# Performance work log

Measured on AMD Instinct MI355X. Metric: run time of the kernel, lower is better.

Reference implementation:

```python
import jax, jax.numpy as jnp
import numpy as np

EMG_SAMPLE_RATE = 2000
ROLLOUT_FREQ = 50
LEFT_CTX = 32
RIGHT_CTX = 32
NUM_POSITION_STEPS = 2000  # in EMG samples
OUT_CH = 20


def _interp_linear(x, size, align_corners):
    """x: [..., L] -> [..., size]; matches torch F.interpolate(mode='linear')."""
    L = x.shape[-1]
    if align_corners:
        src = jnp.arange(size, dtype=jnp.float32) * ((L - 1) / max(size - 1, 1))
    else:
        src = (jnp.arange(size, dtype=jnp.float32) + 0.5) * (L / size) - 0.5
        src = jnp.clip(src, 0.0, L - 1)
    lo = jnp.floor(src).astype(jnp.int32)
    hi = jnp.minimum(lo + 1, L - 1)
    w = (src - lo.astype(jnp.float32)).astype(x.dtype)
    return x[..., lo] * (1 - w) + x[..., hi] * w


def setup_inputs() -> dict:
    key = jax.random.key(0)
    ks = jax.random.split(key, 8)
    B, C, T = 32, 16, 8000
    F, K, H = 512, 65, 512
    emg = jax.random.normal(ks[0], (B, C, T), jnp.float32)
    joint_angles = jax.random.normal(ks[1], (B, OUT_CH, T), jnp.float32)
    no_ik_failure = jnp.ones((B, T), dtype=bool)
    conv_w = jax.random.normal(ks[2], (F, C, K), jnp.float32) * 0.05
    conv_b = jnp.zeros((F,), jnp.float32)
    w1 = jax.random.normal(ks[3], (F + OUT_CH, H), jnp.float32) * 0.04
    b1 = jnp.zeros((H,), jnp.float32)
    w2 = jax.random.normal(ks[4], (H, 2 * OUT_CH), jnp.float32) * 0.04
    b2 = jnp.zeros((2 * OUT_CH,), jnp.float32)
    return dict(emg=emg, joint_angles=joint_angles, no_ik_failure=no_ik_failure,
                provide_initial_pos=1, conv_w=conv_w, conv_b=conv_b,
                w1=w1, b1=b1, w2=w2, b2=b2)


def reference(emg, joint_angles, no_ik_failure, provide_initial_pos,
              conv_w, conv_b, w1, b1, w2, b2):
    B, _, T = emg.shape
    initial_pos = joint_angles[:, :, LEFT_CTX]
    if not provide_initial_pos:
        initial_pos = jnp.zeros_like(initial_pos)

    # encoder: valid Conv1d -> [B, F, T - K + 1] = [B, F, T - 64]
    feats = jax.lax.conv_general_dilated(
        emg, conv_w, window_strides=(1,), padding='VALID',
        dimension_numbers=('NCH', 'OIH', 'NCH')) + conv_b[None, :, None]

    seconds = (T - LEFT_CTX - RIGHT_CTX) / EMG_SAMPLE_RATE
    n_time = round(seconds * ROLLOUT_FREQ)          # static python int
    feats = _interp_linear(feats, n_time, align_corners=True)  # [B, F, n_time]
    num_pos_steps = round(NUM_POSITION_STEPS * (ROLLOUT_FREQ / EMG_SAMPLE_RATE))

    feats_t = jnp.transpose(feats, (2, 0, 1))  # [n_time, B, F]

    def step(prev, inp):
        x_t, t = inp
        # state_condition=True: concat previous pose prediction
        h = jax.nn.relu(jnp.concatenate([x_t, prev], axis=-1) @ w1 + b1)
        out = h @ w2 + b2                       # [B, 2*OUT_CH]
        pos, vel = out[:, :OUT_CH], out[:, OUT_CH:]
        pred = jnp.where(t < num_pos_steps, pos, prev + vel)
        return pred, pred

    _, preds = jax.lax.scan(step, initial_pos,
                            (feats_t, jnp.arange(n_time)))
    pred = jnp.transpose(preds, (1, 2, 0))  # [B, OUT_CH, n_time]

    ja = joint_angles[:, :, LEFT_CTX:T - RIGHT_CTX]
    mask = no_ik_failure[:, LEFT_CTX:T - RIGHT_CTX]
    nt = ja.shape[-1]
    pred_up = _interp_linear(pred, nt, align_corners=False)
    # nearest resample of mask to its own length is identity
    return pred_up, ja, mask
```

## Files before the change

### kernel.cpp

```cpp
#include <hip/hip_runtime.h>

#define NT   198
#define BB   32
#define CC   16
#define TT   8000
#define FF   512
#define KW   65
#define HD   512
#define OUT  20
#define CJ   (CC*KW)
#define KP   1056
#define MM   (NT*BB)
#define TOUT 7936
#define NPS  50

typedef float f4 __attribute__((ext_vector_type(4)));

#define WS_CW 0
#define WS_BX (WS_CW + KP*HD)
#define WS_X  (WS_BX + HD)
#define WS_PR (WS_X  + MM*HD)
#define WS_ET (WS_PR + MM*OUT)
#define WS_W2T (WS_ET + KP*MM)

__device__ __forceinline__ void gll16(const float* g, float* l) {
    __builtin_amdgcn_global_load_lds(
        (const __attribute__((address_space(1))) unsigned int*)g,
        (__attribute__((address_space(3))) unsigned int*)l,
        16, 0, 0);
}

#define XBAR() do { asm volatile("s_waitcnt lgkmcnt(0)" ::: "memory"); \
                    __builtin_amdgcn_s_barrier(); } while (0)

#define ESPAN 2688
#define NB_E  (3 * (BB * CC + 4))
#define NB_CW (((KP + 63) / 64) * (HD / 64))
__global__ __launch_bounds__(256) void k_pre(const float* __restrict__ emg,
                                             const float* __restrict__ cwraw,
                                             const float* __restrict__ w1,
                                             const float* __restrict__ conv_b,
                                             const float* __restrict__ b1,
                                             const float* __restrict__ w2,
                                             float* __restrict__ Et,
                                             float* __restrict__ CW,
                                             float* __restrict__ bX,
                                             float* __restrict__ w2t) {
    __shared__ float sh[2 * 32 * 68];
    const int bid = blockIdx.x;
    const int tid = threadIdx.x;

    if (bid < NB_E) {
        const int bx = bid % (BB * CC + 4);
        const int tc = bid / (BB * CC + 4);
        if (bx >= BB * CC) {
            int idx = (bx - BB * CC) * 3 + tc;
            f4* zp = (f4*)(Et + (size_t)CJ * MM);
            f4 z = {0.f, 0.f, 0.f, 0.f};
            for (int j = tid; j < 2112; j += 256) zp[(size_t)idx * 2112 + j] = z;
            return;
        }
        float* lds_e = sh;
        const int bq = bx >> 4, c = bx & 15;
        const int t0 = tc * 66;
        const float CSTEP = 7935.0f / 197.0f;
        const int elo0 = (int)floorf((float)t0 * CSTEP);
        const float* erow = emg + (size_t)(bq * CC + c) * TT;
        for (int i = tid; i < ESPAN; i += 256) {
            int g = elo0 + i;
            lds_e[i] = erow[(g < TT) ? g : (TT - 1)];
        }
        __syncthreads();
        for (int o = tid; o < 65 * 66; o += 256) {
            int j = o / 66;
            int tl = o - j * 66;
            int t = t0 + tl;
            float src = (float)t * CSTEP;
            float fl = floorf(src);
            int lo = (int)fl;
            float w = src - fl;
            int dhi = (w > 0.f && lo < TOUT - 1) ? 1 : 0;
            int li = lo - elo0 + j;
            float v = (1.0f - w) * lds_e[li] + w * lds_e[li + dhi];
            Et[(size_t)(c * KW + j) * MM + bq * NT + t] = v;
        }
    } else if (bid < NB_E + NB_CW) {
        const int cb = bid - NB_E;
        const int m0 = (cb % 17) * 64;
        const int n0 = (cb / 17) * 64;
        float (*As)[68] = (float(*)[68])sh;
        float (*Bs)[68] = (float(*)[68])(sh + 32 * 68);
        const int tx = tid & 15, ty = tid >> 4;
        const int am = tid & 63;
        const int kb8 = (tid >> 6) * 8;
        const int mrow = m0 + am;
        const int mclamp = mrow < CJ ? mrow : CJ - 1;

        f4 acc[4] = {};
        for (int k0 = 0; k0 < FF; k0 += 32) {
            __syncthreads();
            #pragma unroll
            for (int s = 0; s < 8; ++s)
                As[kb8 + s][am] = cwraw[(size_t)(k0 + kb8 + s) * CJ + mclamp];
            {
                int kb = tid >> 4, c4 = tid & 15;
                *(f4*)&Bs[kb][c4 * 4]      = *(const f4*)(w1 + (size_t)(k0 + kb) * HD + n0 + c4 * 4);
                *(f4*)&Bs[kb + 16][c4 * 4] = *(const f4*)(w1 + (size_t)(k0 + kb + 16) * HD + n0 + c4 * 4);
            }
            __syncthreads();
            #pragma unroll
            for (int kk = 0; kk < 32; ++kk) {
                f4 a = *(f4*)&As[kk][ty * 4];
                f4 bq = *(f4*)&Bs[kk][tx * 4];
                acc[0] += a[0] * bq; acc[1] += a[1] * bq;
                acc[2] += a[2] * bq; acc[3] += a[3] * bq;
            }
        }
        #pragma unroll
        for (int i = 0; i < 4; ++i) {
            int r = m0 + ty * 4 + i;
            if (r < CJ) {
                *(f4*)(CW + (size_t)r * HD + n0 + tx * 4) = acc[i];
            } else if (r < KP) {
                f4 z = {0.f, 0.f, 0.f, 0.f};
                *(f4*)(CW + (size_t)r * HD + n0 + tx * 4) = z;
            }
        }
    } else {
        const int sb = bid - NB_E - NB_CW;
        if (sb < 2) {
            int h = sb * 256 + tid;
            float acc = b1[h];
            for (int f = 0; f < FF; ++f) acc += conv_b[f] * w1[f * HD + h];
            bX[h] = acc;
        } else {
            int q = sb - 2;
            w2t[(size_t)q * HD + tid]       = w2[(size_t)tid * (2 * OUT) + q];
            w2t[(size_t)q * HD + 256 + tid] = w2[(size_t)(256 + tid) * (2 * OUT) + q];
        }
    }
}

__global__ __launch_bounds__(128) void k_x13(const float* __restrict__ Et,
                                             const float* __restrict__ CW,
                                             const float* __restrict__ bX,
                                             float* __restrict__ X0,
                                             float* __restrict__ X1,
                                             float* __restrict__ X2,
                                             float* __restrict__ X3) {
    __shared__ float As[32][64];
    __shared__ float Bs[32][128];
    const int m0 = blockIdx.x * 64;
    const int n0 = blockIdx.y * 128;
    const int kc = blockIdx.z;
    const int kbase = kc * 256;
    const int NK = (kc == 3) ? 9 : 8;
    const int tid = threadIdx.x;
    const int tm = tid >> 4;
    const int tn = tid & 15;
    const int wv = tid >> 6;
    const int lane = tid & 63;

    f4 acc0[8] = {}, acc1[8] = {};

    for (int kt = 0; kt < NK; ++kt) {
        const int k0 = kbase + kt * 32;
        __syncthreads();
        #pragma unroll
        for (int i = 0; i < 4; ++i) {
            int ii = wv * 4 + i;
            const float* src = Et + (size_t)(k0 + 4 * ii + (lane >> 4)) * MM
                             + m0 + (lane & 15) * 4;
            gll16(src, &As[4 * ii][0]);
        }
        #pragma unroll
        for (int j = 0; j < 8; ++j) {
            int jj = wv * 8 + j;
            const float* src = CW + (size_t)(k0 + 2 * jj + (lane >> 5)) * HD
                             + n0 + (lane & 31) * 4;
            gll16(src, &Bs[2 * jj][0]);
        }
        __syncthreads();
        #pragma unroll
        for (int kk = 0; kk < 32; ++kk) {
            f4 a0 = *(const f4*)&As[kk][tm * 8];
            f4 a1 = *(const f4*)&As[kk][tm * 8 + 4];
            f4 b0 = *(const f4*)&Bs[kk][tn * 4];
            f4 b1 = *(const f4*)&Bs[kk][64 + tn * 4];
            #pragma unroll
            for (int i = 0; i < 4; ++i) {
                acc0[i]     += a0[i] * b0;  acc1[i]     += a0[i] * b1;
                acc0[i + 4] += a1[i] * b0;  acc1[i + 4] += a1[i] * b1;
            }
        }
    }

    float* Xo = (kc == 0) ? X0 : (kc == 1) ? X1 : (kc == 2) ? X2 : X3;
    if (kc == 0) {
        f4 bx0 = *(const f4*)(bX + n0 + tn * 4);
        f4 bx1 = *(const f4*)(bX + n0 + 64 + tn * 4);
        #pragma unroll
        for (int i = 0; i < 8; ++i) {
            size_t off = (size_t)(m0 + 8 * tm + i) * HD + n0;
            *(f4*)(Xo + off + tn * 4)      = acc0[i] + bx0;
            *(f4*)(Xo + off + 64 + tn * 4) = acc1[i] + bx1;
        }
    } else {
        #pragma unroll
        for (int i = 0; i < 8; ++i) {
            size_t off = (size_t)(m0 + 8 * tm + i) * HD + n0;
            *(f4*)(Xo + off + tn * 4)      = acc0[i];
            *(f4*)(Xo + off + 64 + tn * 4) = acc1[i];
        }
    }
}

__global__ __launch_bounds__(256) void k_sum4(float* __restrict__ X0,
                                              const float* __restrict__ X1,
                                              const float* __restrict__ X2,
                                              const float* __restrict__ X3) {
    size_t i = (size_t)blockIdx.x * 256 + threadIdx.x;
    f4 a = ((const f4*)X0)[i];
    f4 b = ((const f4*)X1)[i];
    f4 c = ((const f4*)X2)[i];
    f4 d = ((const f4*)X3)[i];
    ((f4*)X0)[i] = (a + b) + (c + d);
}

#define DPPADD(x, ctrl) ((x) + __int_as_float(__builtin_amdgcn_mov_dpp(__float_as_int(x), (ctrl), 0xf, 0xf, true)))

#define SCAN_STEP(T, ISPOS) { \
    if (aown) { \
        int tp = (T) + 2; if (tp > NT - 1) tp = NT - 1; \
        float2 xf = *(const float2*)(Xr + (size_t)tp * HD); \
        f4 pp[5]; \
        _Pragma("unroll") \
        for (int g = 0; g < 5; ++g) pp[g] = *(const f4*)&prev_lds[(T) & 1][g * 4]; \
        float h0a = xc.x, h0b = 0.f, h1a = xc.y, h1b = 0.f; \
        _Pragma("unroll") \
        for (int j = 0; j < 10; ++j) { \
            float pj = pp[j >> 2][j & 3]; \
            h0a = fmaf(pj, w1p[j].x, h0a); h1a = fmaf(pj, w1p[j].y, h1a); } \
        _Pragma("unroll") \
        for (int j = 10; j < OUT; ++j) { \
            float pj = pp[j >> 2][j & 3]; \
            h0b = fmaf(pj, w1p[j].x, h0b); h1b = fmaf(pj, w1p[j].y, h1b); } \
        float h0 = fmaxf(h0a + h0b, 0.f), h1 = fmaxf(h1a + h1b, 0.f); \
        float2 hw; hw.x = h0; hw.y = h1; \
        *(float2*)&h_lds[(T) & 1][tid >> 4][(2 * tid) & 31] = hw; \
        xc = xn; xn = xf; \
    } \
    XBAR(); \
    f4 alo = {0.f, 0.f, 0.f, 0.f}, ahi = {0.f, 0.f, 0.f, 0.f}; \
    _Pragma("unroll") \
    for (int s = 0; s < 4; ++s) { \
        f4 hv0 = *(const f4*)&h_lds[(T) & 1][r][s * 4]; \
        f4 hv1 = *(const f4*)&h_lds[(T) & 1][r][(s + 4) * 4]; \
        alo += hv0 * ((ISPOS) ? wqp[s] : wqv[s]); \
        ahi += hv1 * ((ISPOS) ? wqp[s + 4] : wqv[s + 4]); } \
    f4 a = alo + ahi; \
    float sum = (a[0] + a[1]) + (a[2] + a[3]); \
    sum = DPPADD(sum, 0xB1);    \
    sum = DPPADD(sum, 0x4E);    \
    sum = DPPADD(sum, 0x141);   \
    sum = DPPADD(sum, 0x140);   \
    float outv = sum + ((ISPOS) ? b2p : b2v); \
    myq = (ISPOS) ? outv : (myq + outv); \
    if (r == 0) { \
        predrow[(size_t)(T) * OUT + q] = myq; \
        prev_lds[((T) + 1) & 1][q] = myq; } \
    XBAR(); }

__global__ __launch_bounds__(320, 1) void k_scan(
        const float* __restrict__ X, const float* __restrict__ w1,
        const float* __restrict__ w2t, const float* __restrict__ b2,
        const float* __restrict__ jang, const int* __restrict__ provide,
        float* __restrict__ preds, const unsigned char* __restrict__ m,
        float* __restrict__ outp) {
    const int bid = blockIdx.x;
    const int tid = threadIdx.x;
    const int NF4 = TOUT / 4;

    if (bid >= BB) {
        int cb = bid - BB;
        if (cb < BB * OUT) {
            f4* op = (f4*)(outp + (size_t)BB * OUT * TOUT + (size_t)cb * TOUT);
            const f4* ip = (const f4*)(jang + (size_t)cb * TT + 32);
            for (int i = tid; i < NF4; i += 320) op[i] = ip[i];
        } else {
            int b = cb - BB * OUT;
            f4* op = (f4*)(outp + (size_t)2 * BB * OUT * TOUT + (size_t)b * TOUT);
            const uchar4* mp = (const uchar4*)(m + (size_t)b * TT + 32);
            for (int i = tid; i < NF4; i += 320) {
                uchar4 mv = mp[i];
                f4 o;
                o[0] = mv.x ? 1.0f : 0.0f; o[1] = mv.y ? 1.0f : 0.0f;
                o[2] = mv.z ? 1.0f : 0.0f; o[3] = mv.w ? 1.0f : 0.0f;
                op[i] = o;
            }
        }
        return;
    }

    __shared__ float h_lds[2][16][36];
    __shared__ __align__(16) float prev_lds[2][20];
    const int b = bid;
    const int q = tid >> 4;
    const int r = tid & 15;
    const bool aown = tid < 256;

    float2 w1p[OUT];
    if (aown) {
        #pragma unroll
        for (int j = 0; j < OUT; ++j)
            w1p[j] = *(const float2*)(w1 + (size_t)(FF + j) * HD + 2 * tid);
    }
    f4 wqp[8], wqv[8];
    #pragma unroll
    for (int s = 0; s < 8; ++s) {
        wqp[s] = *(const f4*)(w2t + (size_t)q * HD + r * 32 + s * 4);
        wqv[s] = *(const f4*)(w2t + (size_t)(OUT + q) * HD + r * 32 + s * 4);
    }
    float b2p = b2[q], b2v = b2[OUT + q];

    float pvf = provide[0] ? 1.0f : 0.0f;
    float myq = pvf * jang[(size_t)(b * OUT + q) * TT + 32];
    if (r == 0) prev_lds[0][q] = myq;

    const float* Xr = X + (size_t)b * NT * HD + 2 * tid;
    float* predrow = preds + (size_t)b * NT * OUT;
    float2 xc = {0.f, 0.f}, xn = {0.f, 0.f};
    if (aown) {
        xc = *(const float2*)(Xr);
        xn = *(const float2*)(Xr + HD);
    }
    XBAR();

    __builtin_amdgcn_s_setprio(1);
    for (int t = 0; t < NPS; ++t) { SCAN_STEP(t, true) }
    for (int t = NPS; t < NT; ++t) { SCAN_STEP(t, false) }
    __builtin_amdgcn_s_setprio(0);
}

__global__ __launch_bounds__(256) void k_up(const float* __restrict__ preds,
                                            float* __restrict__ outp) {
    __shared__ float row[NT];
    const int rc = blockIdx.x;
    const int tid = threadIdx.x;
    const int NF4 = TOUT / 4;
    int bq = rc / OUT, ch = rc - bq * OUT;
    if (tid < NT) row[tid] = preds[(size_t)(bq * NT + tid) * OUT + ch];
    __syncthreads();
    const float scale = (float)NT / (float)TOUT;
    f4* op = (f4*)(outp + (size_t)rc * TOUT);
    for (int i = tid; i < NF4; i += 256) {
        f4 o;
        #pragma unroll
        for (int e = 0; e < 4; ++e) {
            int idx = 4 * i + e;
            float src = ((float)idx + 0.5f) * scale - 0.5f;
            src = fminf(fmaxf(src, 0.0f), (float)(NT - 1));
            float fl = floorf(src);
            int lo = (int)fl;
            int hi = lo + 1; if (hi > NT - 1) hi = NT - 1;
            float w = src - fl;
            o[e] = row[lo] * (1.0f - w) + row[hi] * w;
        }
        op[i] = o;
    }
}

extern "C" void kernel_launch(void* const* d_in, const int* in_sizes, int n_in,
                              void* d_out, int out_size, void* d_ws, size_t ws_size,
                              hipStream_t stream) {
    const float* emg     = (const float*)d_in[0];
    const float* jang    = (const float*)d_in[1];
    const unsigned char* msk = (const unsigned char*)d_in[2];
    const int*   provide = (const int*)d_in[3];
    const float* conv_w  = (const float*)d_in[4];
    const float* conv_b  = (const float*)d_in[5];
    const float* w1      = (const float*)d_in[6];
    const float* b1      = (const float*)d_in[7];
    const float* w2      = (const float*)d_in[8];
    const float* b2      = (const float*)d_in[9];
    float* out = (float*)d_out;
    float* ws  = (float*)d_ws;

    float* CW    = ws + WS_CW;
    float* bX    = ws + WS_BX;
    float* X0    = ws + WS_X;
    float* preds = ws + WS_PR;
    float* Et    = ws + WS_ET;
    float* w2t   = ws + WS_W2T;
    float* X1    = out;
    float* X2    = out + (size_t)MM * HD;
    float* X3    = out + (size_t)2 * MM * HD;

    hipLaunchKernelGGL(k_pre,  dim3(NB_E + NB_CW + 42), dim3(256), 0, stream,
                       emg, conv_w, w1, conv_b, b1, w2, Et, CW, bX, w2t);
    hipLaunchKernelGGL(k_x13,  dim3(MM / 64, HD / 128, 4), dim3(128), 0, stream,
                       Et, CW, bX, X0, X1, X2, X3);
    hipLaunchKernelGGL(k_sum4, dim3(MM * HD / 4 / 256), dim3(256), 0, stream,
                       X0, X1, X2, X3);
    hipLaunchKernelGGL(k_scan, dim3(BB + 2 * BB * OUT + BB - BB * OUT), dim3(320), 0, stream,
                       X0, w1, w2t, b2, jang, provide, preds, msk, out);
    hipLaunchKernelGGL(k_up,   dim3(BB * OUT), dim3(256), 0, stream, preds, out);
}
```

Baseline: 251.4 us.

## Overlap recurrent scan with tail of split-K GEMM via per-row-block flags

Replaces the four-way split-K GEMM, the separate sum kernel and the scan with a three-way split-K GEMM followed by a fused kernel. In that kernel the 32 scan blocks start at once and spin on per-M-block completion counters, while the remaining GEMM tiles and the output copies run alongside them. The scan sums the three partial products on the fly, removing the k_sum4 pass, and GEMM tiles are ordered so that early time rows finish first. This adds spin-waiting, extra workspace and reliance on co-residency of the blocks. The old path stays as a fallback when the workspace is too small.

```diff
diff --git a/kernel.cpp b/kernel.cpp
--- a/kernel.cpp
+++ b/kernel.cpp
@@ -22,6 +22,10 @@
 #define WS_PR (WS_X  + MM*HD)
 #define WS_ET (WS_PR + MM*OUT)
 #define WS_W2T (WS_ET + KP*MM)
+#define WS_X4 (WS_W2T + 2*OUT*HD)
+#define WS_X5 (WS_X4 + MM*HD)
+#define WS_FLG (WS_X5 + MM*HD)
+#define WS_NEED_BIG ((size_t)(WS_FLG + 128) * 4)
 
 __device__ __forceinline__ void gll16(const float* g, float* l) {
     __builtin_amdgcn_global_load_lds(
@@ -45,7 +49,9 @@
                                              float* __restrict__ Et,
                                              float* __restrict__ CW,
                                              float* __restrict__ bX,
-                                             float* __restrict__ w2t) {
+                                             float* __restrict__ w2t,
+                                             int* __restrict__ flags,
+                                             int do_flags) {
     __shared__ float sh[2 * 32 * 68];
     const int bid = blockIdx.x;
     const int tid = threadIdx.x;
@@ -133,10 +139,315 @@
             float acc = b1[h];
             for (int f = 0; f < FF; ++f) acc += conv_b[f] * w1[f * HD + h];
             bX[h] = acc;
-        } else {
+        } else if (sb < 42) {
             int q = sb - 2;
             w2t[(size_t)q * HD + tid]       = w2[(size_t)tid * (2 * OUT) + q];
             w2t[(size_t)q * HD + 256 + tid] = w2[(size_t)(256 + tid) * (2 * OUT) + q];
+        } else {
+            if (do_flags && tid < 128) flags[tid] = 0;
+        }
+    }
+}
+
+__device__ __forceinline__ int rank_to_mx(int r) {
+    int jr = (r < 31) ? (68 + r) : (r - 31);
+    return (jr * 65) % 99;
+}
+
+__global__ __launch_bounds__(128) void k_g1(const float* __restrict__ Et,
+                                            const float* __restrict__ CW,
+                                            const float* __restrict__ bX,
+                                            float* __restrict__ X0,
+                                            float* __restrict__ X1,
+                                            float* __restrict__ X2,
+                                            int* __restrict__ flags) {
+    __shared__ float As[32 * 64];
+    __shared__ float Bs[32 * 128];
+    const int g = blockIdx.x;
+    const int r = g / 12;
+    const int rem = g - r * 12;
+    const int mx = rank_to_mx(r);
+    const int ny = rem & 3, kc = rem >> 2;
+    const int m0 = mx * 64;
+    const int n0 = ny * 128;
+    const int kbase = kc * 352;
+    const int tid = threadIdx.x;
+    const int tm = tid >> 4, tn = tid & 15;
+    const int wv = tid >> 6, lane = tid & 63;
+
+    f4 acc0[8] = {}, acc1[8] = {};
+    for (int kt = 0; kt < 11; ++kt) {
+        const int k0 = kbase + kt * 32;
+        __syncthreads();
+        #pragma unroll
+        for (int i = 0; i < 4; ++i) {
+            int ii = wv * 4 + i;
+            gll16(Et + (size_t)(k0 + 4 * ii + (lane >> 4)) * MM + m0 + (lane & 15) * 4,
+                  As + (4 * ii) * 64);
+        }
+        #pragma unroll
+        for (int j = 0; j < 8; ++j) {
+            int jj = wv * 8 + j;
+            gll16(CW + (size_t)(k0 + 2 * jj + (lane >> 5)) * HD + n0 + (lane & 31) * 4,
+                  Bs + (2 * jj) * 128);
+        }
+        __syncthreads();
+        #pragma unroll
+        for (int kk = 0; kk < 32; ++kk) {
+            f4 a0 = *(const f4*)&As[kk * 64 + tm * 8];
+            f4 a1 = *(const f4*)&As[kk * 64 + tm * 8 + 4];
+            f4 b0 = *(const f4*)&Bs[kk * 128 + tn * 4];
+            f4 b1 = *(const f4*)&Bs[kk * 128 + 64 + tn * 4];
+            #pragma unroll
+            for (int i = 0; i < 4; ++i) {
+                acc0[i]     += a0[i] * b0;  acc1[i]     += a0[i] * b1;
+                acc0[i + 4] += a1[i] * b0;  acc1[i + 4] += a1[i] * b1;
+            }
+        }
+    }
+    float* Xo = (kc == 0) ? X0 : (kc == 1) ? X1 : X2;
+    if (kc == 0) {
+        f4 bx0 = *(const f4*)(bX + n0 + tn * 4);
+        f4 bx1 = *(const f4*)(bX + n0 + 64 + tn * 4);
+        #pragma unroll
+        for (int i = 0; i < 8; ++i) {
+            size_t off = (size_t)(m0 + 8 * tm + i) * HD + n0;
+            *(f4*)(Xo + off + tn * 4)      = acc0[i] + bx0;
+            *(f4*)(Xo + off + 64 + tn * 4) = acc1[i] + bx1;
+        }
+    } else {
+        #pragma unroll
+        for (int i = 0; i < 8; ++i) {
+            size_t off = (size_t)(m0 + 8 * tm + i) * HD + n0;
+            *(f4*)(Xo + off + tn * 4)      = acc0[i];
+            *(f4*)(Xo + off + 64 + tn * 4) = acc1[i];
+        }
+    }
+    __threadfence();
+    __syncthreads();
+    if (tid == 0) atomicAdd(flags + mx, 1);
+}
+
+#define DPPADD(x, ctrl) ((x) + __int_as_float(__builtin_amdgcn_mov_dpp(__float_as_int(x), (ctrl), 0xf, 0xf, true)))
+
+#define SCAN_STEP3(T, ISPOS) { \
+    if (aown) { \
+        int tp = (T) + 2; if (tp > NT - 1) tp = NT - 1; \
+        int mbf = (b * NT + tp) >> 6; \
+        while (mbdone < mbf) { \
+            int nx = mbdone + 1; \
+            while (__hip_atomic_load(fl + nx, __ATOMIC_ACQUIRE, __HIP_MEMORY_SCOPE_AGENT) < 12) \
+                __builtin_amdgcn_s_sleep(8); \
+            mbdone = nx; } \
+        float2 xfa = *(const float2*)(Xr0 + (size_t)tp * HD); \
+        float2 xfb = *(const float2*)(Xr1 + (size_t)tp * HD); \
+        float2 xfc = *(const float2*)(Xr2 + (size_t)tp * HD); \
+        float2 xf; xf.x = (xfa.x + xfb.x) + xfc.x; xf.y = (xfa.y + xfb.y) + xfc.y; \
+        f4 pp[5]; \
+        _Pragma("unroll") \
+        for (int g = 0; g < 5; ++g) pp[g] = *(const f4*)&prev_lds[((T) & 1) * 20 + g * 4]; \
+        float h0a = xc.x, h0b = 0.f, h1a = xc.y, h1b = 0.f; \
+        _Pragma("unroll") \
+        for (int j = 0; j < 10; ++j) { \
+            float pj = pp[j >> 2][j & 3]; \
+            h0a = fmaf(pj, w1p[j].x, h0a); h1a = fmaf(pj, w1p[j].y, h1a); } \
+        _Pragma("unroll") \
+        for (int j = 10; j < OUT; ++j) { \
+            float pj = pp[j >> 2][j & 3]; \
+            h0b = fmaf(pj, w1p[j].x, h0b); h1b = fmaf(pj, w1p[j].y, h1b); } \
+        float h0 = fmaxf(h0a + h0b, 0.f), h1 = fmaxf(h1a + h1b, 0.f); \
+        float2 hw; hw.x = h0; hw.y = h1; \
+        *(float2*)&h_lds[(T) & 1][tid >> 4][(2 * tid) & 31] = hw; \
+        xc = xn; xn = xf; \
+    } \
+    XBAR(); \
+    f4 alo = {0.f, 0.f, 0.f, 0.f}, ahi = {0.f, 0.f, 0.f, 0.f}; \
+    _Pragma("unroll") \
+    for (int s = 0; s < 4; ++s) { \
+        f4 hv0 = *(const f4*)&h_lds[(T) & 1][r][s * 4]; \
+        f4 hv1 = *(const f4*)&h_lds[(T) & 1][r][(s + 4) * 4]; \
+        alo += hv0 * ((ISPOS) ? wqp[s] : wqv[s]); \
+        ahi += hv1 * ((ISPOS) ? wqp[s + 4] : wqv[s + 4]); } \
+    f4 a = alo + ahi; \
+    float sum = (a[0] + a[1]) + (a[2] + a[3]); \
+    sum = DPPADD(sum, 0xB1); \
+    sum = DPPADD(sum, 0x4E); \
+    sum = DPPADD(sum, 0x141); \
+    sum = DPPADD(sum, 0x140); \
+    float outv = sum + ((ISPOS) ? b2p : b2v); \
+    myq = (ISPOS) ? outv : (myq + outv); \
+    if (r == 0) { \
+        predrow[(size_t)(T) * OUT + q] = myq; \
+        prev_lds[(((T) + 1) & 1) * 20 + q] = myq; } \
+    XBAR(); }
+
+__global__ __launch_bounds__(320, 1) void k_main(
+        const float* __restrict__ X0, const float* __restrict__ X1,
+        const float* __restrict__ X2, const float* __restrict__ Et,
+        const float* __restrict__ CW, const float* __restrict__ bX,
+        const float* __restrict__ w1, const float* __restrict__ w2t,
+        const float* __restrict__ b2, const float* __restrict__ jang,
+        const int* __restrict__ provide, float* __restrict__ preds,
+        const unsigned char* __restrict__ m, float* __restrict__ outp,
+        int* __restrict__ flags,
+        float* __restrict__ X0w, float* __restrict__ X1w, float* __restrict__ X2w) {
+    __shared__ float sh[12288];
+    const int bid = blockIdx.x;
+    const int tid = threadIdx.x;
+    const int NF4 = TOUT / 4;
+
+    if (bid < BB) {
+        float (*h_lds)[16][36] = (float(*)[16][36])sh;
+        float* prev_lds = sh + 1152;
+        const int b = bid;
+        const int q = tid >> 4;
+        const int r = tid & 15;
+        const bool aown = tid < 256;
+        const int* fl = flags;
+
+        float2 w1p[OUT];
+        if (aown) {
+            #pragma unroll
+            for (int j = 0; j < OUT; ++j)
+                w1p[j] = *(const float2*)(w1 + (size_t)(FF + j) * HD + 2 * tid);
+        }
+        f4 wqp[8], wqv[8];
+        #pragma unroll
+        for (int s = 0; s < 8; ++s) {
+            wqp[s] = *(const f4*)(w2t + (size_t)q * HD + r * 32 + s * 4);
+            wqv[s] = *(const f4*)(w2t + (size_t)(OUT + q) * HD + r * 32 + s * 4);
+        }
+        float b2p = b2[q], b2v = b2[OUT + q];
+
+        float pvf = provide[0] ? 1.0f : 0.0f;
+        float myq = pvf * jang[(size_t)(b * OUT + q) * TT + 32];
+        if (r == 0) prev_lds[0 * 20 + q] = myq;
+
+        const float* Xr0 = X0 + (size_t)b * NT * HD + 2 * tid;
+        const float* Xr1 = X1 + (size_t)b * NT * HD + 2 * tid;
+        const float* Xr2 = X2 + (size_t)b * NT * HD + 2 * tid;
+        float* predrow = preds + (size_t)b * NT * OUT;
+        float2 xc = {0.f, 0.f}, xn = {0.f, 0.f};
+        int mbdone = ((b * NT) >> 6) - 1;
+        if (aown) {
+            int mbf = (b * NT + 1) >> 6;
+            while (mbdone < mbf) {
+                int nx = mbdone + 1;
+                while (__hip_atomic_load(fl + nx, __ATOMIC_ACQUIRE, __HIP_MEMORY_SCOPE_AGENT) < 12)
+                    __builtin_amdgcn_s_sleep(8);
+                mbdone = nx;
+            }
+            float2 a0 = *(const float2*)(Xr0);
+            float2 a1 = *(const float2*)(Xr1);
+            float2 a2 = *(const float2*)(Xr2);
+            xc.x = (a0.x + a1.x) + a2.x; xc.y = (a0.y + a1.y) + a2.y;
+            float2 c0 = *(const float2*)(Xr0 + HD);
+            float2 c1 = *(const float2*)(Xr1 + HD);
+            float2 c2 = *(const float2*)(Xr2 + HD);
+            xn.x = (c0.x + c1.x) + c2.x; xn.y = (c0.y + c1.y) + c2.y;
+        }
+        XBAR();
+
+        for (int t = 0; t < NPS; ++t) { SCAN_STEP3(t, true) }
+        for (int t = NPS; t < NT; ++t) { SCAN_STEP3(t, false) }
+        return;
+    }
+
+    if (bid < BB + 240) {
+        const bool gwork = tid < 256;
+        const int half = (tid >> 7) & 1;
+        const int ltid = tid & 127;
+        const int g2 = bid - BB;
+        const int v = 708 + 2 * g2 + half;
+        const int rr = v / 12;
+        const int rem = v - rr * 12;
+        const int mx = rank_to_mx(rr);
+        const int ny = rem & 3, kc = rem >> 2;
+        const int m0 = mx * 64;
+        const int n0 = ny * 128;
+        const int kbase = kc * 352;
+        float* As = sh + half * 6144;
+        float* Bs = As + 2048;
+        const int tm = ltid >> 4, tn = ltid & 15;
+        const int wv = ltid >> 6, lane = ltid & 63;
+
+        f4 acc0[8] = {}, acc1[8] = {};
+        for (int kt = 0; kt < 11; ++kt) {
+            const int k0 = kbase + kt * 32;
+            __syncthreads();
+            if (gwork) {
+                #pragma unroll
+                for (int i = 0; i < 4; ++i) {
+                    int ii = wv * 4 + i;
+                    gll16(Et + (size_t)(k0 + 4 * ii + (lane >> 4)) * MM + m0 + (lane & 15) * 4,
+                          As + (4 * ii) * 64);
+                }
+                #pragma unroll
+                for (int j = 0; j < 8; ++j) {
+                    int jj = wv * 8 + j;
+                    gll16(CW + (size_t)(k0 + 2 * jj + (lane >> 5)) * HD + n0 + (lane & 31) * 4,
+                          Bs + (2 * jj) * 128);
+                }
+            }
+            __syncthreads();
+            if (gwork) {
+                #pragma unroll
+                for (int kk = 0; kk < 32; ++kk) {
+                    f4 a0 = *(const f4*)&As[kk * 64 + tm * 8];
+                    f4 a1 = *(const f4*)&As[kk * 64 + tm * 8 + 4];
+                    f4 b0 = *(const f4*)&Bs[kk * 128 + tn * 4];
+                    f4 b1 = *(const f4*)&Bs[kk * 128 + 64 + tn * 4];
+                    #pragma unroll
+                    for (int i = 0; i < 4; ++i) {
+                        acc0[i]     += a0[i] * b0;  acc1[i]     += a0[i] * b1;
+                        acc0[i + 4] += a1[i] * b0;  acc1[i + 4] += a1[i] * b1;
+                    }
+                }
+            }
+        }
+        if (gwork) {
+            float* Xo = (kc == 0) ? X0w : (kc == 1) ? X1w : X2w;
+            if (kc == 0) {
+                f4 bx0 = *(const f4*)(bX + n0 + tn * 4);
+                f4 bx1 = *(const f4*)(bX + n0 + 64 + tn * 4);
+                #pragma unroll
+                for (int i = 0; i < 8; ++i) {
+                    size_t off = (size_t)(m0 + 8 * tm + i) * HD + n0;
+                    *(f4*)(Xo + off + tn * 4)      = acc0[i] + bx0;
+                    *(f4*)(Xo + off + 64 + tn * 4) = acc1[i] + bx1;
+                }
+            } else {
+                #pragma unroll
+                for (int i = 0; i < 8; ++i) {
+                    size_t off = (size_t)(m0 + 8 * tm + i) * HD + n0;
+                    *(f4*)(Xo + off + tn * 4)      = acc0[i];
+                    *(f4*)(Xo + off + 64 + tn * 4) = acc1[i];
+                }
+            }
+        }
+        __threadfence();
+        __syncthreads();
+        if (gwork && ltid == 0) atomicAdd(flags + mx, 1);
+        return;
+    }
+
+    {
+        int cb = bid - (BB + 240);
+        if (cb < BB * OUT) {
+            f4* op = (f4*)(outp + (size_t)BB * OUT * TOUT + (size_t)cb * TOUT);
+            const f4* ip = (const f4*)(jang + (size_t)cb * TT + 32);
+            for (int i = tid; i < NF4; i += 320) op[i] = ip[i];
+        } else {
+            int b = cb - BB * OUT;
+            f4* op = (f4*)(outp + (size_t)2 * BB * OUT * TOUT + (size_t)b * TOUT);
+            const uchar4* mp = (const uchar4*)(m + (size_t)b * TT + 32);
+            for (int i = tid; i < NF4; i += 320) {
+                uchar4 mv = mp[i];
+                f4 o;
+                o[0] = mv.x ? 1.0f : 0.0f; o[1] = mv.y ? 1.0f : 0.0f;
+                o[2] = mv.z ? 1.0f : 0.0f; o[3] = mv.w ? 1.0f : 0.0f;
+                op[i] = o;
+            }
         }
     }
 }
@@ -156,29 +467,24 @@
     const int kbase = kc * 256;
     const int NK = (kc == 3) ? 9 : 8;
     const int tid = threadIdx.x;
-    const int tm = tid >> 4;
-    const int tn = tid & 15;
-    const int wv = tid >> 6;
-    const int lane = tid & 63;
+    const int tm = tid >> 4, tn = tid & 15;
+    const int wv = tid >> 6, lane = tid & 63;
 
     f4 acc0[8] = {}, acc1[8] = {};
-
     for (int kt = 0; kt < NK; ++kt) {
         const int k0 = kbase + kt * 32;
         __syncthreads();
         #pragma unroll
         for (int i = 0; i < 4; ++i) {
             int ii = wv * 4 + i;
-            const float* src = Et + (size_t)(k0 + 4 * ii + (lane >> 4)) * MM
-                             + m0 + (lane & 15) * 4;
-            gll16(src, &As[4 * ii][0]);
+            gll16(Et + (size_t)(k0 + 4 * ii + (lane >> 4)) * MM + m0 + (lane & 15) * 4,
+                  &As[4 * ii][0]);
         }
         #pragma unroll
         for (int j = 0; j < 8; ++j) {
             int jj = wv * 8 + j;
-            const float* src = CW + (size_t)(k0 + 2 * jj + (lane >> 5)) * HD
-                             + n0 + (lane & 31) * 4;
-            gll16(src, &Bs[2 * jj][0]);
+            gll16(CW + (size_t)(k0 + 2 * jj + (lane >> 5)) * HD + n0 + (lane & 31) * 4,
+                  &Bs[2 * jj][0]);
         }
         __syncthreads();
         #pragma unroll
@@ -194,7 +500,6 @@
             }
         }
     }
-
     float* Xo = (kc == 0) ? X0 : (kc == 1) ? X1 : (kc == 2) ? X2 : X3;
     if (kc == 0) {
         f4 bx0 = *(const f4*)(bX + n0 + tn * 4);
@@ -226,8 +531,6 @@
     f4 d = ((const f4*)X3)[i];
     ((f4*)X0)[i] = (a + b) + (c + d);
 }
-
-#define DPPADD(x, ctrl) ((x) + __int_as_float(__builtin_amdgcn_mov_dpp(__float_as_int(x), (ctrl), 0xf, 0xf, true)))
 
 #define SCAN_STEP(T, ISPOS) { \
     if (aown) { \
@@ -260,10 +563,10 @@
         ahi += hv1 * ((ISPOS) ? wqp[s + 4] : wqv[s + 4]); } \
     f4 a = alo + ahi; \
     float sum = (a[0] + a[1]) + (a[2] + a[3]); \
-    sum = DPPADD(sum, 0xB1);    \
-    sum = DPPADD(sum, 0x4E);    \
-    sum = DPPADD(sum, 0x141);   \
-    sum = DPPADD(sum, 0x140);   \
+    sum = DPPADD(sum, 0xB1); \
+    sum = DPPADD(sum, 0x4E); \
+    sum = DPPADD(sum, 0x141); \
+    sum = DPPADD(sum, 0x140); \
     float outv = sum + ((ISPOS) ? b2p : b2v); \
     myq = (ISPOS) ? outv : (myq + outv); \
     if (r == 0) { \
@@ -271,7 +574,7 @@
         prev_lds[((T) + 1) & 1][q] = myq; } \
     XBAR(); }
 
-__global__ __launch_bounds__(320, 1) void k_scan(
+__global__ __launch_bounds__(320, 1) void k_scan_fb(
         const float* __restrict__ X, const float* __restrict__ w1,
         const float* __restrict__ w2t, const float* __restrict__ b2,
         const float* __restrict__ jang, const int* __restrict__ provide,
@@ -336,10 +639,8 @@
     }
     XBAR();
 
-    __builtin_amdgcn_s_setprio(1);
     for (int t = 0; t < NPS; ++t) { SCAN_STEP(t, true) }
     for (int t = NPS; t < NT; ++t) { SCAN_STEP(t, false) }
-    __builtin_amdgcn_s_setprio(0);
 }
 
 __global__ __launch_bounds__(256) void k_up(const float* __restrict__ preds,
@@ -392,17 +693,31 @@
     float* preds = ws + WS_PR;
     float* Et    = ws + WS_ET;
     float* w2t   = ws + WS_W2T;
-    float* X1    = out;
-    float* X2    = out + (size_t)MM * HD;
-    float* X3    = out + (size_t)2 * MM * HD;
-
-    hipLaunchKernelGGL(k_pre,  dim3(NB_E + NB_CW + 42), dim3(256), 0, stream,
-                       emg, conv_w, w1, conv_b, b1, w2, Et, CW, bX, w2t);
-    hipLaunchKernelGGL(k_x13,  dim3(MM / 64, HD / 128, 4), dim3(128), 0, stream,
-                       Et, CW, bX, X0, X1, X2, X3);
-    hipLaunchKernelGGL(k_sum4, dim3(MM * HD / 4 / 256), dim3(256), 0, stream,
-                       X0, X1, X2, X3);
-    hipLaunchKernelGGL(k_scan, dim3(BB + 2 * BB * OUT + BB - BB * OUT), dim3(320), 0, stream,
-                       X0, w1, w2t, b2, jang, provide, preds, msk, out);
-    hipLaunchKernelGGL(k_up,   dim3(BB * OUT), dim3(256), 0, stream, preds, out);
-}
+
+    const int big = (ws_size >= WS_NEED_BIG) ? 1 : 0;
+    int* flags = (int*)(ws + WS_FLG);
+
+    hipLaunchKernelGGL(k_pre, dim3(NB_E + NB_CW + 43), dim3(256), 0, stream,
+                       emg, conv_w, w1, conv_b, b1, w2, Et, CW, bX, w2t, flags, big);
+
+    if (big) {
+        float* X1w = ws + WS_X4;
+        float* X2w = ws + WS_X5;
+        hipLaunchKernelGGL(k_g1, dim3(708), dim3(128), 0, stream,
+                           Et, CW, bX, X0, X1w, X2w, flags);
+        hipLaunchKernelGGL(k_main, dim3(BB + 240 + 672), dim3(320), 0, stream,
+                           X0, X1w, X2w, Et, CW, bX, w1, w2t, b2, jang, provide,
+                           preds, msk, out, flags, X0, X1w, X2w);
+    } else {
+        float* X1 = out;
+        float* X2 = out + (size_t)MM * HD;
+        float* X3 = out + (size_t)2 * MM * HD;
+        hipLaunchKernelGGL(k_x13, dim3(MM / 64, HD / 128, 4), dim3(128), 0, stream,
+                           Et, CW, bX, X0, X1, X2, X3);
+        hipLaunchKernelGGL(k_sum4, dim3(MM * HD / 4 / 256), dim3(256), 0, stream,
+                           X0, X1, X2, X3);
+        hipLaunchKernelGGL(k_scan_fb, dim3(BB + 2 * BB * OUT + BB - BB * OUT), dim3(320), 0, stream,
+                           X0, w1, w2t, b2, jang, provide, preds, msk, out);
+    }
+    hipLaunchKernelGGL(k_up, dim3(BB * OUT), dim3(256), 0, stream, preds, out);
+}
```

Result: slower. 304.5 us (+21.1%).
